# Kernel tuning notes

Measured on AMD Instinct MI355X. Metric: run time of the kernel, lower is better.

Reference implementation:

```python
import jax, jax.numpy as jnp
import numpy as np

B, D, L = 16, 256, 200
T = 1000   # max_frame_length
K = 3      # kernel_size
DW, DC = 4, 2


def setup_inputs() -> dict:
    key = jax.random.key(0)
    ks = jax.random.split(key, 16)
    plen = jax.random.randint(ks[0], (B,), 150, L + 1)
    pm = jnp.arange(L)[None, :] < plen[:, None]              # (B,L) True=valid
    phoneme_mask = pm[:, None, :]                            # (B,1,L)
    durations = jax.random.uniform(ks[1], (B, L), minval=1.0, maxval=8.0) * pm
    phoneme = jax.random.normal(ks[2], (B, D, L), dtype=jnp.float32)
    s = 0.05
    params = {
        'Wpw': jax.random.normal(ks[3], (D, D)) * s, 'bpw': jnp.zeros((D,)),
        'Cw': jax.random.normal(ks[4], (8, D, K)) * s, 'cbw': jnp.zeros((8,)),
        'Mw': jax.random.normal(ks[5], (10, DW)) * s, 'mbw': jnp.zeros((DW,)),
        'Lw': jax.random.normal(ks[6], (DW * D, D)) * s, 'lbw': jnp.zeros((D,)),
        'Wpc': jax.random.normal(ks[7], (D, D)) * s, 'bpc': jnp.zeros((D,)),
        'Cc': jax.random.normal(ks[8], (8, D, K)) * s, 'cbc': jnp.zeros((8,)),
        'Mc': jax.random.normal(ks[9], (10, DC)) * s, 'mbc': jnp.zeros((DC,)),
        'Lc': jax.random.normal(ks[10], (DW * DC, D)) * s, 'lbc': jnp.zeros((D,)),
        'Wo': jax.random.normal(ks[11], (D, 2 * D)) * s, 'bo': jnp.zeros((2 * D,)),
    }
    return {'durations': durations, 'phoneme': phoneme, 'phoneme_mask': phoneme_mask, **params}


def _conv_swish(x, W1, b1, Ck, cb, pm):
    # 1x1 conv (proj) then kernel-K 'same' conv then SiLU; mask padded phones
    h = jnp.einsum('od,bdl->bol', W1, x) + b1[None, :, None]
    h = jax.lax.conv_general_dilated(h, Ck, (1,), 'SAME',
                                     dimension_numbers=('NCH', 'OIH', 'NCH')) + cb[None, :, None]
    h = jax.nn.silu(h)
    h = jnp.where(pm[:, None, :], h, 0.0)
    return h.transpose(0, 2, 1)  # (B, L, 8)


def _mlp(S, E, h, M, mb):
    # concat start/end boundary scalars with per-phone conv features -> (B,T,L,10)
    feat = jnp.concatenate([S[..., None], E[..., None],
                            jnp.broadcast_to(h[:, None], (B, T, L, 8))], axis=-1)
    return jax.nn.silu(feat @ M + mb)


def _forward(durations, phoneme, phoneme_mask, Wpw, bpw, Cw, cbw, Mw, mbw, Lw, lbw,
             Wpc, bpc, Cc, cbc, Mc, mbc, Lc, lbc, Wo, bo):
    pm = phoneme_mask[:, 0, :]                                          # (B,L)
    frame_lengths = jnp.clip(jnp.round(durations.sum(-1)).astype(jnp.int32), 0, T)
    frame_mask = jnp.arange(T)[None, :] < frame_lengths[:, None]        # (B,T)
    attn_mask = frame_mask[:, :, None] & pm[:, None, :]                 # (B,T,L)
    sd = jnp.cumsum(durations, axis=-1)                                 # (B,L)
    sk = sd - durations
    t = jnp.arange(1, T + 1, dtype=durations.dtype)
    S = jnp.where(attn_mask, t[None, :, None] - sk[:, None, :], 0.0)    # (B,T,L)
    E = jnp.where(attn_mask, (sd - sk)[:, None, :], 0.0)                # (B,T,L)

    h_w = _conv_swish(phoneme, Wpw, bpw, Cw, cbw, pm)
    w = _mlp(S, E, h_w, Mw, mbw)                                        # (B,T,L,DW)
    w = jnp.where(pm[:, None, :, None], w, -jnp.inf)
    w = jax.nn.softmax(w, axis=2)                                       # softmax over phones
    w = jnp.where(frame_mask[:, :, None, None], w, 0.0)

    h_c = _conv_swish(phoneme, Wpc, bpc, Cc, cbc, pm)
    c = _mlp(S, E, h_c, Mc, mbc)                                        # (B,T,L,DC)

    wh = jnp.einsum('btlq,bdl->btqd', w, phoneme).reshape(B, T, DW * D) @ Lw + lbw
    wc = jnp.einsum('btlq,btlp->btqp', w, c).reshape(B, T, DW * DC) @ Lc + lbc
    whc = jnp.where(frame_mask[..., None], wh + wc, 0.0)                # (B,T,D)
    out = (whc @ Wo + bo).transpose(0, 2, 1)                            # (B,2D,T)
    return out, frame_mask, frame_lengths, w.transpose(0, 3, 1, 2)


def reference(durations, phoneme, phoneme_mask, Wpw, bpw, Cw, cbw, Mw, mbw, Lw, lbw,
              Wpc, bpc, Cc, cbc, Mc, mbc, Lc, lbc, Wo, bo):
    out, frame_mask, frame_lengths, w = _forward(
        durations, phoneme, phoneme_mask, Wpw, bpw, Cw, cbw, Mw, mbw, Lw, lbw,
        Wpc, bpc, Cc, cbc, Mc, mbc, Lc, lbc, Wo, bo)
    mean, log_std = jnp.split(out, 2, axis=1)                           # (B,D,T) each
    return (mean, log_std, frame_mask, frame_lengths, w)
```

## Files before the change

### kernel.cpp

```cpp
#include <hip/hip_runtime.h>
#include <hip/hip_bf16.h>
#include <math.h>

#define NB 16
#define ND 256
#define NL 200
#define NT 1000

typedef unsigned short ushort_t;
typedef __bf16 bf16x8 __attribute__((ext_vector_type(8)));
typedef float f32x4 __attribute__((ext_vector_type(4)));

#define LDS_AS(p) ((__attribute__((address_space(3))) void*)(p))
#define GLB_AS(p) ((const __attribute__((address_space(1))) void*)(p))

#define OFF_PHT   0u
#define OFF_SK    4966400u
#define OFF_EW    4969600u
#define OFF_EC    4975744u
#define OFF_BW2   4981888u
#define OFF_BC2   4981912u
#define OFF_FL    4981936u
#define OFF_GT    11535552u
#define OFF_WHC   13173952u
#define OFF_WOT   15221952u
#define OFF_BASE  15287488u
#define OFF_PHTB  15320256u
#define OFF_LWT   15844544u

__device__ __forceinline__ float silu_f(float x){ return x / (1.f + __expf(-x)); }
__device__ __forceinline__ ushort_t f2bf(float x){
  __hip_bfloat16 h = __float2bfloat16(x);
  return *(ushort_t*)&h;
}

__global__ __launch_bounds__(256) void k_stage1(
    const float* __restrict__ dur, const float* __restrict__ ph,
    const float* __restrict__ Wp_w, const float* __restrict__ C_w, const float* __restrict__ bp_w,
    const float* __restrict__ Wp_c, const float* __restrict__ C_c, const float* __restrict__ bp_c,
    const float* __restrict__ Wo, const float* __restrict__ Lw,
    float* __restrict__ sk_ws, int* __restrict__ fl_ws,
    float* __restrict__ o_fm, float* __restrict__ o_fl,
    float* __restrict__ Ew, float* __restrict__ Ec,
    float* __restrict__ bw2, float* __restrict__ bc2,
    ushort_t* __restrict__ WoT, ushort_t* __restrict__ LwT,
    float* __restrict__ phT, ushort_t* __restrict__ phTb)
{
  int bid = blockIdx.x, tid = threadIdx.x;
  if (bid < 16){
    int b = bid;
    __shared__ float sdur[NL];
    __shared__ float ssk[NL];
    __shared__ int sfl;
    if (tid < NL) sdur[tid] = dur[b*NL + tid];
    __syncthreads();
    if (tid == 0){
      float run = 0.f;
      for (int l = 0; l < NL; ++l){ ssk[l] = run; run += sdur[l]; }
      int fl = (int)rintf(run);
      fl = fl < 0 ? 0 : (fl > NT ? NT : fl);
      sfl = fl; fl_ws[b] = fl; o_fl[b] = (float)fl;
    }
    __syncthreads();
    if (tid < NL) sk_ws[b*NL + tid] = ssk[tid];
    for (int t = tid; t < NT; t += 256) o_fm[b*NT + t] = (t < sfl) ? 1.f : 0.f;
  } else if (bid < 1600){
    int sbid = bid - 16;
    if (sbid < 48){
      int gid = sbid*256 + tid;
      int branch = gid / 6144;
      int r = gid % 6144;
      int d = r & 255;
      int ock = r >> 8;
      int oc = ock / 3, k = ock % 3;
      const float* Wp = branch ? Wp_c : Wp_w;
      const float* C  = branch ? C_c  : C_w;
      float acc = 0.f;
      for (int i = 0; i < ND; ++i) acc += C[(oc*ND + i)*3 + k] * Wp[i*ND + d];
      (branch ? Ec : Ew)[r] = acc;
      if (d == 0){
        const float* bp = branch ? bp_c : bp_w;
        float bb = 0.f;
        for (int i = 0; i < ND; ++i) bb += C[(oc*ND + i)*3 + k] * bp[i];
        (branch ? bc2 : bw2)[ock] = bb;
      }
    } else {
      int gid = (sbid - 48)*256 + tid;
      if (gid < 131072){
        int n = gid >> 8, k = gid & 255;
        WoT[gid] = f2bf(Wo[(size_t)k*512 + n]);
      } else {
        int r = gid - 131072;
        int d = r & 255;
        int qn = r >> 8;
        int q = qn >> 8, n = qn & 255;
        LwT[r] = f2bf(Lw[((size_t)q*256 + d)*256 + n]);
      }
    }
  } else {
    int r = bid - 1600;
    int xb = r & 7, yb = (r >> 3) & 7, b = r >> 6;
    int l0 = xb*32, d0 = yb*32;
    int tx = tid & 31, ty = tid >> 5;
    __shared__ float tile[32][33];
    #pragma unroll
    for (int i = 0; i < 4; ++i){
      int d = d0 + ty + i*8, l = l0 + tx;
      tile[ty + i*8][tx] = (l < NL) ? ph[((size_t)b*ND + d)*NL + l] : 0.f;
    }
    __syncthreads();
    #pragma unroll
    for (int i = 0; i < 4; ++i){
      int l = l0 + ty + i*8, d = d0 + tx;
      float v = tile[tx][ty + i*8];
      if (l < NL) phT[((size_t)b*NL + l)*ND + d] = v;
      phTb[((size_t)b*256 + l)*ND + d] = f2bf(v);
    }
  }
}

__global__ __launch_bounds__(256) void k_stage2(
    const float* __restrict__ phT,
    const float* __restrict__ dur, const float* __restrict__ sk_ws,
    const float* __restrict__ Ew, const float* __restrict__ Ec,
    const float* __restrict__ bw2, const float* __restrict__ bc2,
    const float* __restrict__ cbw, const float* __restrict__ cbc,
    const float* __restrict__ Mw, const float* __restrict__ mbw,
    const float* __restrict__ Mc, const float* __restrict__ mbc,
    float4* __restrict__ base,
    const ushort_t* __restrict__ LwT, const ushort_t* __restrict__ phTb,
    ushort_t* __restrict__ Gt)
{
  int bid = blockIdx.x, tid = threadIdx.x;
  if (bid < 256){
    int b = bid >> 4, x = bid & 15;
    if (x >= 13){
      int l0 = 208 + (x - 13)*16;
      if (tid < 32)
        base[((size_t)(b*256 + l0 + (tid >> 1)))*2 + (tid & 1)] = make_float4(0,0,0,0);
      return;
    }
    __shared__ float sh[16][17];
    int lu = tid >> 4, u = tid & 15;
    int l = x*16 + lu;
    float h = 0.f;
    if (l < NL){
      int branch = u >> 3, oc = u & 7;
      const float* E  = branch ? Ec  : Ew;
      const float* b2 = branch ? bc2 : bw2;
      float val = (branch ? cbc : cbw)[oc];
      #pragma unroll
      for (int k = 0; k < 3; ++k){
        int ll = l + k - 1;
        if (ll < 0 || ll >= NL) continue;
        float acc = b2[oc*3 + k];
        const float4* Er = (const float4*)(E + (oc*3 + k)*ND);
        const float4* pr = (const float4*)(phT + ((size_t)b*NL + ll)*ND);
        #pragma unroll 8
        for (int d = 0; d < 64; ++d){
          float4 e = Er[d], p = pr[d];
          acc += e.x*p.x + e.y*p.y + e.z*p.z + e.w*p.w;
        }
        val += acc;
      }
      float pm = (dur[b*NL + l] > 0.5f) ? 1.f : 0.f;
      h = silu_f(val) * pm;
    }
    sh[lu][u] = h;
    __syncthreads();
    if (tid < 16){
      int ll = x*16 + tid;
      float4 o0 = make_float4(0,0,0,0);
      float4 o1 = make_float4(0,0,0,0);
      if (ll < NL){
        float dl  = dur[b*NL + ll];
        float pm  = (dl > 0.5f) ? 1.f : 0.f;
        float skl = sk_ws[b*NL + ll];
        float c1[4], c2[2];
        #pragma unroll
        for (int q = 0; q < 4; ++q) c1[q] = mbw[q] + dl*Mw[4 + q] - skl*Mw[q];
        #pragma unroll
        for (int p = 0; p < 2; ++p) c2[p] = mbc[p] + dl*Mc[2 + p] - skl*Mc[p];
        #pragma unroll
        for (int j = 0; j < 8; ++j){
          float hwv = sh[tid][j], hcv = sh[tid][8 + j];
          #pragma unroll
          for (int q = 0; q < 4; ++q) c1[q] += hwv*Mw[(2 + j)*4 + q];
          #pragma unroll
          for (int p = 0; p < 2; ++p) c2[p] += hcv*Mc[(2 + j)*2 + p];
        }
        o0 = make_float4(c1[0], c1[1], c1[2], c1[3]);
        o1 = make_float4(c2[0], c2[1], pm, 0.f);
      }
      base[((size_t)(b*256 + ll))*2 + 0] = o0;
      base[((size_t)(b*256 + ll))*2 + 1] = o1;
    }
  } else {
    int r = bid - 256;
    int xb = r & 1, yb = (r >> 1) & 1, bq = r >> 2;
    int b = bq >> 2, q = bq & 3;
    int m0 = yb * 128;
    int n0 = xb * 128;
    int lane = tid & 63, wave = tid >> 6;
    int wm = wave >> 1, wn = wave & 1;
    int col = lane & 15, kg4 = lane >> 4;
    f32x4 acc[4][4] = {};
    for (int kt = 0; kt < 8; ++kt){
      int k0 = kt*32;
      bf16x8 afr[4], bfr[4];
      #pragma unroll
      for (int i = 0; i < 4; ++i)
        afr[i] = *(const bf16x8*)(LwT + ((size_t)(q*256 + m0 + wm*64 + i*16 + col))*256 + k0 + kg4*8);
      #pragma unroll
      for (int j = 0; j < 4; ++j)
        bfr[j] = *(const bf16x8*)(phTb + ((size_t)(b*256 + n0 + wn*64 + j*16 + col))*256 + k0 + kg4*8);
      #pragma unroll
      for (int i = 0; i < 4; ++i)
        #pragma unroll
        for (int j = 0; j < 4; ++j)
          acc[i][j] = __builtin_amdgcn_mfma_f32_16x16x32_bf16(afr[i], bfr[j], acc[i][j], 0, 0, 0);
    }
    int rq = lane >> 4;
    #pragma unroll
    for (int i = 0; i < 4; ++i){
      #pragma unroll
      for (int rr = 0; rr < 4; ++rr){
        int n = m0 + wm*64 + i*16 + rq*4 + rr;
        #pragma unroll
        for (int j = 0; j < 4; ++j){
          int l = n0 + wn*64 + j*16 + col;
          if (l < NL)
            Gt[((size_t)b*ND + n)*800 + q*NL + l] = f2bf(acc[i][j][rr]);
        }
      }
    }
  }
}

#define AP 808
__global__ __launch_bounds__(256) void k_wv_fused(
    const float4* __restrict__ base,
    const int* __restrict__ fl_ws,
    const float* __restrict__ Mw, const float* __restrict__ Mc,
    const ushort_t* __restrict__ Gt,
    const float* __restrict__ Lc,
    const float* __restrict__ lbc,
    const float* __restrict__ lbw,
    float* __restrict__ wout,
    ushort_t* __restrict__ whc)
{
  __shared__ ushort_t As[32*AP];
  __shared__ float    wcs[32][8];
  int b = blockIdx.y;
  int m0 = blockIdx.x * 32;
  int tid = threadIdx.x, lane = tid & 63, wave = tid >> 6;
  int col = lane & 15, kg4 = lane >> 4;
  int fl = fl_ws[b];

  for (int s = 0; s < 8; ++s){
    int tl = wave*8 + s;
    int t = m0 + tl;
    if (t >= fl){
      for (int k = lane; k < 800; k += 64) As[tl*AP + k] = 0;
      if (lane < 8) wcs[tl][lane] = 0.f;
      if (t < NT){
        #pragma unroll
        for (int q = 0; q < 4; ++q)
          #pragma unroll
          for (int c = 0; c < 4; ++c){
            int l = c*64 + lane;
            if (l < NL) wout[(((size_t)(b*4 + q))*NT + t)*NL + l] = 0.f;
          }
      }
      continue;
    }
    float t1 = (float)(t + 1);
    float tqw[4], tqc[2];
    #pragma unroll
    for (int q = 0; q < 4; ++q) tqw[q] = t1 * Mw[q];
    #pragma unroll
    for (int p = 0; p < 2; ++p) tqc[p] = t1 * Mc[p];
    float z[4][4], cv[4][2], msk[4];
    float m[4] = {-INFINITY, -INFINITY, -INFINITY, -INFINITY};
    #pragma unroll
    for (int c = 0; c < 4; ++c){
      int l = c*64 + lane;
      float4 b0 = base[((size_t)(b*256 + l))*2 + 0];
      float4 b1 = base[((size_t)(b*256 + l))*2 + 1];
      float pm = b1.z;
      msk[c] = pm;
      float zz[4] = { b0.x + tqw[0], b0.y + tqw[1], b0.z + tqw[2], b0.w + tqw[3] };
      #pragma unroll
      for (int q = 0; q < 4; ++q){
        float sv = silu_f(zz[q]);
        z[c][q] = (pm > 0.f) ? sv : -INFINITY;
        m[q] = fmaxf(m[q], z[c][q]);
      }
      cv[c][0] = silu_f(b1.x + tqc[0]);
      cv[c][1] = silu_f(b1.y + tqc[1]);
    }
    #pragma unroll
    for (int q = 0; q < 4; ++q){
      float v = m[q];
      #pragma unroll
      for (int off = 32; off; off >>= 1) v = fmaxf(v, __shfl_xor(v, off));
      m[q] = v;
    }
    float s4[4] = {0,0,0,0};
    #pragma unroll
    for (int c = 0; c < 4; ++c){
      #pragma unroll
      for (int q = 0; q < 4; ++q){
        float e = (msk[c] > 0.f) ? __expf(z[c][q] - m[q]) : 0.f;
        z[c][q] = e;
        s4[q] += e;
      }
    }
    #pragma unroll
    for (int q = 0; q < 4; ++q){
      float v = s4[q];
      #pragma unroll
      for (int off = 32; off; off >>= 1) v += __shfl_xor(v, off);
      s4[q] = 1.f / v;
    }
    float wc[8] = {0,0,0,0,0,0,0,0};
    #pragma unroll
    for (int c = 0; c < 4; ++c){
      int l = c*64 + lane;
      bool lv = l < NL;
      #pragma unroll
      for (int q = 0; q < 4; ++q){
        float wq = z[c][q] * s4[q];
        if (lv){
          wout[(((size_t)(b*4 + q))*NT + t)*NL + l] = wq;
          As[tl*AP + q*NL + l] = f2bf(wq);
        }
        wc[q*2 + 0] += wq * cv[c][0];
        wc[q*2 + 1] += wq * cv[c][1];
      }
    }
    #pragma unroll
    for (int u = 0; u < 8; ++u){
      float v = wc[u];
      #pragma unroll
      for (int off = 32; off; off >>= 1) v += __shfl_xor(v, off);
      wc[u] = v;
    }
    if (lane == 0){
      #pragma unroll
      for (int u = 0; u < 8; ++u) wcs[tl][u] = wc[u];
    }
  }
  __syncthreads();

  f32x4 acc[2][4] = {};
  const ushort_t* Gb = Gt + (size_t)b*ND*800;
  for (int kt = 0; kt < 25; ++kt){
    int k0 = kt*32;
    bf16x8 afr[2], bfr[4];
    #pragma unroll
    for (int i = 0; i < 2; ++i)
      afr[i] = *(const bf16x8*)(&As[(i*16 + col)*AP + k0 + kg4*8]);
    #pragma unroll
    for (int j = 0; j < 4; ++j)
      bfr[j] = *(const bf16x8*)(Gb + ((size_t)(wave*64 + j*16 + col))*800 + k0 + kg4*8);
    #pragma unroll
    for (int i = 0; i < 2; ++i)
      #pragma unroll
      for (int j = 0; j < 4; ++j)
        acc[i][j] = __builtin_amdgcn_mfma_f32_16x16x32_bf16(afr[i], bfr[j], acc[i][j], 0, 0, 0);
  }

  int rq = lane >> 4;
  float lcn[4][8], lbn[4], lbwn[4];
  #pragma unroll
  for (int j = 0; j < 4; ++j){
    int n = wave*64 + j*16 + col;
    lbn[j] = lbc[n]; lbwn[j] = lbw[n];
    #pragma unroll
    for (int u = 0; u < 8; ++u) lcn[j][u] = Lc[u*ND + n];
  }
  #pragma unroll
  for (int i = 0; i < 2; ++i){
    #pragma unroll
    for (int r = 0; r < 4; ++r){
      int tl = i*16 + rq*4 + r;
      int t = m0 + tl;
      if (t >= NT) continue;
      float f = (t < fl) ? 1.f : 0.f;
      #pragma unroll
      for (int j = 0; j < 4; ++j){
        float vcv = lbn[j]
          + wcs[tl][0]*lcn[j][0] + wcs[tl][1]*lcn[j][1]
          + wcs[tl][2]*lcn[j][2] + wcs[tl][3]*lcn[j][3]
          + wcs[tl][4]*lcn[j][4] + wcs[tl][5]*lcn[j][5]
          + wcs[tl][6]*lcn[j][6] + wcs[tl][7]*lcn[j][7];
        int n = wave*64 + j*16 + col;
        whc[((size_t)b*NT + t)*ND + n] = f2bf(f * (acc[i][j][r] + lbwn[j] + vcv));
      }
    }
  }
}

__global__ __launch_bounds__(256) void k_gemmO_mfma(
    const ushort_t* __restrict__ whc,
    const ushort_t* __restrict__ WoT,
    const float* __restrict__ bo,
    float* __restrict__ o_mean, float* __restrict__ o_lstd)
{
  int m0 = blockIdx.y * 128;
  int n0 = blockIdx.x * 128;
  int tid = threadIdx.x, lane = tid & 63, wave = tid >> 6;
  int wm = wave >> 1, wn = wave & 1;
  int col = lane & 15, kg4 = lane >> 4;

  f32x4 acc[4][4] = {};

  for (int kt = 0; kt < 8; ++kt){
    int k0 = kt*32;
    bf16x8 afr[4], bfr[4];
    #pragma unroll
    for (int i = 0; i < 4; ++i)
      afr[i] = *(const bf16x8*)(WoT + ((size_t)(m0 + wm*64 + i*16 + col))*ND + k0 + kg4*8);
    #pragma unroll
    for (int j = 0; j < 4; ++j)
      bfr[j] = *(const bf16x8*)(whc + ((size_t)(n0 + wn*64 + j*16 + col))*ND + k0 + kg4*8);
    #pragma unroll
    for (int i = 0; i < 4; ++i)
      #pragma unroll
      for (int j = 0; j < 4; ++j)
        acc[i][j] = __builtin_amdgcn_mfma_f32_16x16x32_bf16(afr[i], bfr[j], acc[i][j], 0, 0, 0);
  }

  int rq = lane >> 4;
  #pragma unroll
  for (int i = 0; i < 4; ++i){
    #pragma unroll
    for (int r = 0; r < 4; ++r){
      int s = m0 + wm*64 + i*16 + rq*4 + r;
      float bov = bo[s];
      #pragma unroll
      for (int j = 0; j < 4; ++j){
        int bt = n0 + wn*64 + j*16 + col;
        int b = bt / NT, t = bt - b*NT;
        float v = acc[i][j][r] + bov;
        if (s < ND) o_mean[((size_t)b*ND + s)*NT + t] = v;
        else        o_lstd[((size_t)b*ND + (s - ND))*NT + t] = v;
      }
    }
  }
}

extern "C" void kernel_launch(void* const* d_in, const int* in_sizes, int n_in,
                              void* d_out, int out_size, void* d_ws, size_t ws_size,
                              hipStream_t stream)
{
  const float* dur = (const float*)d_in[0];
  const float* ph  = (const float*)d_in[1];
  const float* Wpw = (const float*)d_in[3];
  const float* bpw = (const float*)d_in[4];
  const float* Cw  = (const float*)d_in[5];
  const float* cbw = (const float*)d_in[6];
  const float* Mw  = (const float*)d_in[7];
  const float* mbw = (const float*)d_in[8];
  const float* Lw  = (const float*)d_in[9];
  const float* lbw = (const float*)d_in[10];
  const float* Wpc = (const float*)d_in[11];
  const float* bpc = (const float*)d_in[12];
  const float* Cc  = (const float*)d_in[13];
  const float* cbc = (const float*)d_in[14];
  const float* Mc  = (const float*)d_in[15];
  const float* mbc = (const float*)d_in[16];
  const float* Lc  = (const float*)d_in[17];
  const float* lbc = (const float*)d_in[18];
  const float* Wo  = (const float*)d_in[19];
  const float* bo  = (const float*)d_in[20];

  float* out    = (float*)d_out;
  float* o_mean = out;
  float* o_lstd = out + (size_t)NB*ND*NT;
  float* o_fm   = o_lstd + (size_t)NB*ND*NT;
  float* o_fl   = o_fm + NB*NT;
  float* o_w    = o_fl + NB;

  float* ws   = (float*)d_ws;
  float* phT  = ws + OFF_PHT;
  float* sk   = ws + OFF_SK;
  float* Ew   = ws + OFF_EW;
  float* Ec   = ws + OFF_EC;
  float* bw2  = ws + OFF_BW2;
  float* bc2  = ws + OFF_BC2;
  int*   fl   = (int*)(ws + OFF_FL);
  ushort_t* Gt   = (ushort_t*)(ws + OFF_GT);
  ushort_t* whc  = (ushort_t*)(ws + OFF_WHC);
  ushort_t* WoT  = (ushort_t*)(ws + OFF_WOT);
  float4*   base = (float4*)(ws + OFF_BASE);
  ushort_t* phTb = (ushort_t*)(ws + OFF_PHTB);
  ushort_t* LwT  = (ushort_t*)(ws + OFF_LWT);

  k_stage1<<<2624, 256, 0, stream>>>(dur, ph, Wpw, Cw, bpw, Wpc, Cc, bpc, Wo, Lw,
                                     sk, fl, o_fm, o_fl, Ew, Ec, bw2, bc2,
                                     WoT, LwT, phT, phTb);
  k_stage2<<<512, 256, 0, stream>>>(phT, dur, sk, Ew, Ec, bw2, bc2, cbw, cbc,
                                    Mw, mbw, Mc, mbc, base, LwT, phTb, Gt);
  {
    dim3 g(32, NB);
    k_wv_fused<<<g, 256, 0, stream>>>(base, fl, Mw, Mc, Gt, Lc, lbc, lbw,
                                      o_w, whc);
  }
  {
    dim3 g(125, 4);
    k_gemmO_mfma<<<g, 256, 0, stream>>>(whc, WoT, bo, o_mean, o_lstd);
  }
}
```

Before: 254.2 us.

## Fuse four kernel launches into one persistent kernel with grid barriers

Merges the four stage kernels into a single persistent kernel of 512 blocks that separates stages with a software grid-wide barrier built on atomics, and adds a memset to reset the barrier counter before each launch. Stage 1 work is spread over the blocks with a grid-stride loop. The aim is to remove per-launch overhead and the gaps between kernels. The risks are a deadlock if all 512 blocks cannot be resident at once (the code requests 2 blocks per CU through launch bounds and uses about 52 KB of shared memory per block), the cost of the barrier spin itself, and lost occupancy in later stages where only some blocks have work.

```diff
diff --git a/kernel.cpp b/kernel.cpp
--- a/kernel.cpp
+++ b/kernel.cpp
@@ -6,13 +6,12 @@
 #define ND 256
 #define NL 200
 #define NT 1000
+#define NBLK 512
+#define AP 808
 
 typedef unsigned short ushort_t;
 typedef __bf16 bf16x8 __attribute__((ext_vector_type(8)));
 typedef float f32x4 __attribute__((ext_vector_type(4)));
-
-#define LDS_AS(p) ((__attribute__((address_space(3))) void*)(p))
-#define GLB_AS(p) ((const __attribute__((address_space(1))) void*)(p))
 
 #define OFF_PHT   0u
 #define OFF_SK    4966400u
@@ -21,6 +20,7 @@
 #define OFF_BW2   4981888u
 #define OFF_BC2   4981912u
 #define OFF_FL    4981936u
+#define OFF_BAR   4982000u
 #define OFF_GT    11535552u
 #define OFF_WHC   13173952u
 #define OFF_WOT   15221952u
@@ -34,166 +34,186 @@
   return *(ushort_t*)&h;
 }
 
-__global__ __launch_bounds__(256) void k_stage1(
+__device__ __forceinline__ void grid_sync(unsigned* bar){
+  __syncthreads();
+  if (threadIdx.x == 0){
+    __threadfence();
+    unsigned g = __hip_atomic_load(bar + 1, __ATOMIC_RELAXED, __HIP_MEMORY_SCOPE_AGENT);
+    unsigned my = __hip_atomic_fetch_add(bar, 1u, __ATOMIC_ACQ_REL, __HIP_MEMORY_SCOPE_AGENT);
+    if (my == (unsigned)(NBLK - 1)){
+      __hip_atomic_store(bar, 0u, __ATOMIC_RELAXED, __HIP_MEMORY_SCOPE_AGENT);
+      __hip_atomic_fetch_add(bar + 1, 1u, __ATOMIC_RELEASE, __HIP_MEMORY_SCOPE_AGENT);
+    } else {
+      while (__hip_atomic_load(bar + 1, __ATOMIC_ACQUIRE, __HIP_MEMORY_SCOPE_AGENT) == g)
+        __builtin_amdgcn_s_sleep(2);
+    }
+    __threadfence();
+  }
+  __syncthreads();
+}
+
+__global__ __launch_bounds__(256, 2) void k_all(
     const float* __restrict__ dur, const float* __restrict__ ph,
     const float* __restrict__ Wp_w, const float* __restrict__ C_w, const float* __restrict__ bp_w,
     const float* __restrict__ Wp_c, const float* __restrict__ C_c, const float* __restrict__ bp_c,
     const float* __restrict__ Wo, const float* __restrict__ Lw,
+    const float* __restrict__ cbw, const float* __restrict__ cbc,
+    const float* __restrict__ Mw, const float* __restrict__ mbw,
+    const float* __restrict__ Mc, const float* __restrict__ mbc,
+    const float* __restrict__ Lc, const float* __restrict__ lbc,
+    const float* __restrict__ lbw, const float* __restrict__ bo,
     float* __restrict__ sk_ws, int* __restrict__ fl_ws,
     float* __restrict__ o_fm, float* __restrict__ o_fl,
     float* __restrict__ Ew, float* __restrict__ Ec,
     float* __restrict__ bw2, float* __restrict__ bc2,
     ushort_t* __restrict__ WoT, ushort_t* __restrict__ LwT,
-    float* __restrict__ phT, ushort_t* __restrict__ phTb)
+    float* __restrict__ phT, ushort_t* __restrict__ phTb,
+    float4* __restrict__ base, ushort_t* __restrict__ Gt,
+    float* __restrict__ wout, ushort_t* __restrict__ whc,
+    float* __restrict__ o_mean, float* __restrict__ o_lstd,
+    unsigned* __restrict__ bar)
 {
+  __shared__ __align__(16) unsigned char smem[52736];
   int bid = blockIdx.x, tid = threadIdx.x;
-  if (bid < 16){
-    int b = bid;
-    __shared__ float sdur[NL];
-    __shared__ float ssk[NL];
-    __shared__ int sfl;
-    if (tid < NL) sdur[tid] = dur[b*NL + tid];
+
+  for (int vb = bid; vb < 2624; vb += NBLK){
+    if (vb < 16){
+      int b = vb;
+      float* sdur = (float*)smem;
+      float* ssk  = sdur + 256;
+      int*   sfl  = (int*)(ssk + 256);
+      if (tid < NL) sdur[tid] = dur[b*NL + tid];
+      __syncthreads();
+      if (tid == 0){
+        float run = 0.f;
+        for (int l = 0; l < NL; ++l){ ssk[l] = run; run += sdur[l]; }
+        int fl = (int)rintf(run);
+        fl = fl < 0 ? 0 : (fl > NT ? NT : fl);
+        sfl[0] = fl; fl_ws[b] = fl; o_fl[b] = (float)fl;
+      }
+      __syncthreads();
+      if (tid < NL) sk_ws[b*NL + tid] = ssk[tid];
+      int flv = sfl[0];
+      for (int t = tid; t < NT; t += 256) o_fm[b*NT + t] = (t < flv) ? 1.f : 0.f;
+    } else if (vb < 1600){
+      int sbid = vb - 16;
+      if (sbid < 48){
+        int gid = sbid*256 + tid;
+        int branch = gid / 6144;
+        int r = gid % 6144;
+        int d = r & 255;
+        int ock = r >> 8;
+        int oc = ock / 3, k = ock % 3;
+        const float* Wp = branch ? Wp_c : Wp_w;
+        const float* C  = branch ? C_c  : C_w;
+        float acc = 0.f;
+        for (int i = 0; i < ND; ++i) acc += C[(oc*ND + i)*3 + k] * Wp[i*ND + d];
+        (branch ? Ec : Ew)[r] = acc;
+        if (d == 0){
+          const float* bp = branch ? bp_c : bp_w;
+          float bb = 0.f;
+          for (int i = 0; i < ND; ++i) bb += C[(oc*ND + i)*3 + k] * bp[i];
+          (branch ? bc2 : bw2)[ock] = bb;
+        }
+      } else {
+        int gid = (sbid - 48)*256 + tid;
+        if (gid < 131072){
+          int n = gid >> 8, k = gid & 255;
+          WoT[gid] = f2bf(Wo[(size_t)k*512 + n]);
+        } else {
+          int r = gid - 131072;
+          int d = r & 255;
+          int qn = r >> 8;
+          int q = qn >> 8, n = qn & 255;
+          LwT[r] = f2bf(Lw[((size_t)q*256 + d)*256 + n]);
+        }
+      }
+    } else {
+      int r = vb - 1600;
+      int xb = r & 7, yb = (r >> 3) & 7, b = r >> 6;
+      int l0 = xb*32, d0 = yb*32;
+      int tx = tid & 31, ty = tid >> 5;
+      float (*tile)[33] = (float (*)[33])smem;
+      #pragma unroll
+      for (int i = 0; i < 4; ++i){
+        int d = d0 + ty + i*8, l = l0 + tx;
+        tile[ty + i*8][tx] = (l < NL) ? ph[((size_t)b*ND + d)*NL + l] : 0.f;
+      }
+      __syncthreads();
+      #pragma unroll
+      for (int i = 0; i < 4; ++i){
+        int l = l0 + ty + i*8, d = d0 + tx;
+        float v = tile[tx][ty + i*8];
+        if (l < NL) phT[((size_t)b*NL + l)*ND + d] = v;
+        phTb[((size_t)b*256 + l)*ND + d] = f2bf(v);
+      }
+    }
     __syncthreads();
-    if (tid == 0){
-      float run = 0.f;
-      for (int l = 0; l < NL; ++l){ ssk[l] = run; run += sdur[l]; }
-      int fl = (int)rintf(run);
-      fl = fl < 0 ? 0 : (fl > NT ? NT : fl);
-      sfl = fl; fl_ws[b] = fl; o_fl[b] = (float)fl;
-    }
-    __syncthreads();
-    if (tid < NL) sk_ws[b*NL + tid] = ssk[tid];
-    for (int t = tid; t < NT; t += 256) o_fm[b*NT + t] = (t < sfl) ? 1.f : 0.f;
-  } else if (bid < 1600){
-    int sbid = bid - 16;
-    if (sbid < 48){
-      int gid = sbid*256 + tid;
-      int branch = gid / 6144;
-      int r = gid % 6144;
-      int d = r & 255;
-      int ock = r >> 8;
-      int oc = ock / 3, k = ock % 3;
-      const float* Wp = branch ? Wp_c : Wp_w;
-      const float* C  = branch ? C_c  : C_w;
-      float acc = 0.f;
-      for (int i = 0; i < ND; ++i) acc += C[(oc*ND + i)*3 + k] * Wp[i*ND + d];
-      (branch ? Ec : Ew)[r] = acc;
-      if (d == 0){
-        const float* bp = branch ? bp_c : bp_w;
-        float bb = 0.f;
-        for (int i = 0; i < ND; ++i) bb += C[(oc*ND + i)*3 + k] * bp[i];
-        (branch ? bc2 : bw2)[ock] = bb;
-      }
-    } else {
-      int gid = (sbid - 48)*256 + tid;
-      if (gid < 131072){
-        int n = gid >> 8, k = gid & 255;
-        WoT[gid] = f2bf(Wo[(size_t)k*512 + n]);
-      } else {
-        int r = gid - 131072;
-        int d = r & 255;
-        int qn = r >> 8;
-        int q = qn >> 8, n = qn & 255;
-        LwT[r] = f2bf(Lw[((size_t)q*256 + d)*256 + n]);
-      }
-    }
-  } else {
-    int r = bid - 1600;
-    int xb = r & 7, yb = (r >> 3) & 7, b = r >> 6;
-    int l0 = xb*32, d0 = yb*32;
-    int tx = tid & 31, ty = tid >> 5;
-    __shared__ float tile[32][33];
-    #pragma unroll
-    for (int i = 0; i < 4; ++i){
-      int d = d0 + ty + i*8, l = l0 + tx;
-      tile[ty + i*8][tx] = (l < NL) ? ph[((size_t)b*ND + d)*NL + l] : 0.f;
-    }
-    __syncthreads();
-    #pragma unroll
-    for (int i = 0; i < 4; ++i){
-      int l = l0 + ty + i*8, d = d0 + tx;
-      float v = tile[tx][ty + i*8];
-      if (l < NL) phT[((size_t)b*NL + l)*ND + d] = v;
-      phTb[((size_t)b*256 + l)*ND + d] = f2bf(v);
-    }
   }
-}
-
-__global__ __launch_bounds__(256) void k_stage2(
-    const float* __restrict__ phT,
-    const float* __restrict__ dur, const float* __restrict__ sk_ws,
-    const float* __restrict__ Ew, const float* __restrict__ Ec,
-    const float* __restrict__ bw2, const float* __restrict__ bc2,
-    const float* __restrict__ cbw, const float* __restrict__ cbc,
-    const float* __restrict__ Mw, const float* __restrict__ mbw,
-    const float* __restrict__ Mc, const float* __restrict__ mbc,
-    float4* __restrict__ base,
-    const ushort_t* __restrict__ LwT, const ushort_t* __restrict__ phTb,
-    ushort_t* __restrict__ Gt)
-{
-  int bid = blockIdx.x, tid = threadIdx.x;
+  grid_sync(bar);
+
   if (bid < 256){
     int b = bid >> 4, x = bid & 15;
     if (x >= 13){
       int l0 = 208 + (x - 13)*16;
       if (tid < 32)
         base[((size_t)(b*256 + l0 + (tid >> 1)))*2 + (tid & 1)] = make_float4(0,0,0,0);
-      return;
-    }
-    __shared__ float sh[16][17];
-    int lu = tid >> 4, u = tid & 15;
-    int l = x*16 + lu;
-    float h = 0.f;
-    if (l < NL){
-      int branch = u >> 3, oc = u & 7;
-      const float* E  = branch ? Ec  : Ew;
-      const float* b2 = branch ? bc2 : bw2;
-      float val = (branch ? cbc : cbw)[oc];
-      #pragma unroll
-      for (int k = 0; k < 3; ++k){
-        int ll = l + k - 1;
-        if (ll < 0 || ll >= NL) continue;
-        float acc = b2[oc*3 + k];
-        const float4* Er = (const float4*)(E + (oc*3 + k)*ND);
-        const float4* pr = (const float4*)(phT + ((size_t)b*NL + ll)*ND);
-        #pragma unroll 8
-        for (int d = 0; d < 64; ++d){
-          float4 e = Er[d], p = pr[d];
-          acc += e.x*p.x + e.y*p.y + e.z*p.z + e.w*p.w;
-        }
-        val += acc;
-      }
-      float pm = (dur[b*NL + l] > 0.5f) ? 1.f : 0.f;
-      h = silu_f(val) * pm;
-    }
-    sh[lu][u] = h;
-    __syncthreads();
-    if (tid < 16){
-      int ll = x*16 + tid;
-      float4 o0 = make_float4(0,0,0,0);
-      float4 o1 = make_float4(0,0,0,0);
-      if (ll < NL){
-        float dl  = dur[b*NL + ll];
-        float pm  = (dl > 0.5f) ? 1.f : 0.f;
-        float skl = sk_ws[b*NL + ll];
-        float c1[4], c2[2];
-        #pragma unroll
-        for (int q = 0; q < 4; ++q) c1[q] = mbw[q] + dl*Mw[4 + q] - skl*Mw[q];
-        #pragma unroll
-        for (int p = 0; p < 2; ++p) c2[p] = mbc[p] + dl*Mc[2 + p] - skl*Mc[p];
-        #pragma unroll
-        for (int j = 0; j < 8; ++j){
-          float hwv = sh[tid][j], hcv = sh[tid][8 + j];
+    } else {
+      float (*sh)[17] = (float (*)[17])smem;
+      int lu = tid >> 4, u = tid & 15;
+      int l = x*16 + lu;
+      float h = 0.f;
+      if (l < NL){
+        int branch = u >> 3, oc = u & 7;
+        const float* E  = branch ? Ec  : Ew;
+        const float* b2 = branch ? bc2 : bw2;
+        float val = (branch ? cbc : cbw)[oc];
+        #pragma unroll
+        for (int k = 0; k < 3; ++k){
+          int ll = l + k - 1;
+          if (ll < 0 || ll >= NL) continue;
+          float acc = b2[oc*3 + k];
+          const float4* Er = (const float4*)(E + (oc*3 + k)*ND);
+          const float4* pr = (const float4*)(phT + ((size_t)b*NL + ll)*ND);
+          #pragma unroll 8
+          for (int d = 0; d < 64; ++d){
+            float4 e = Er[d], p = pr[d];
+            acc += e.x*p.x + e.y*p.y + e.z*p.z + e.w*p.w;
+          }
+          val += acc;
+        }
+        float pm = (dur[b*NL + l] > 0.5f) ? 1.f : 0.f;
+        h = silu_f(val) * pm;
+      }
+      sh[lu][u] = h;
+      __syncthreads();
+      if (tid < 16){
+        int ll = x*16 + tid;
+        float4 o0 = make_float4(0,0,0,0);
+        float4 o1 = make_float4(0,0,0,0);
+        if (ll < NL){
+          float dl  = dur[b*NL + ll];
+          float pm  = (dl > 0.5f) ? 1.f : 0.f;
+          float skl = sk_ws[b*NL + ll];
+          float c1[4], c2[2];
           #pragma unroll
-          for (int q = 0; q < 4; ++q) c1[q] += hwv*Mw[(2 + j)*4 + q];
+          for (int q = 0; q < 4; ++q) c1[q] = mbw[q] + dl*Mw[4 + q] - skl*Mw[q];
           #pragma unroll
-          for (int p = 0; p < 2; ++p) c2[p] += hcv*Mc[(2 + j)*2 + p];
-        }
-        o0 = make_float4(c1[0], c1[1], c1[2], c1[3]);
-        o1 = make_float4(c2[0], c2[1], pm, 0.f);
-      }
-      base[((size_t)(b*256 + ll))*2 + 0] = o0;
-      base[((size_t)(b*256 + ll))*2 + 1] = o1;
+          for (int p = 0; p < 2; ++p) c2[p] = mbc[p] + dl*Mc[2 + p] - skl*Mc[p];
+          #pragma unroll
+          for (int j = 0; j < 8; ++j){
+            float hwv = sh[tid][j], hcv = sh[tid][8 + j];
+            #pragma unroll
+            for (int q = 0; q < 4; ++q) c1[q] += hwv*Mw[(2 + j)*4 + q];
+            #pragma unroll
+            for (int p = 0; p < 2; ++p) c2[p] += hcv*Mc[(2 + j)*2 + p];
+          }
+          o0 = make_float4(c1[0], c1[1], c1[2], c1[3]);
+          o1 = make_float4(c2[0], c2[1], pm, 0.f);
+        }
+        base[((size_t)(b*256 + ll))*2 + 0] = o0;
+        base[((size_t)(b*256 + ll))*2 + 1] = o1;
+      }
     }
   } else {
     int r = bid - 256;
@@ -235,217 +255,203 @@
       }
     }
   }
-}
-
-#define AP 808
-__global__ __launch_bounds__(256) void k_wv_fused(
-    const float4* __restrict__ base,
-    const int* __restrict__ fl_ws,
-    const float* __restrict__ Mw, const float* __restrict__ Mc,
-    const ushort_t* __restrict__ Gt,
-    const float* __restrict__ Lc,
-    const float* __restrict__ lbc,
-    const float* __restrict__ lbw,
-    float* __restrict__ wout,
-    ushort_t* __restrict__ whc)
-{
-  __shared__ ushort_t As[32*AP];
-  __shared__ float    wcs[32][8];
-  int b = blockIdx.y;
-  int m0 = blockIdx.x * 32;
-  int tid = threadIdx.x, lane = tid & 63, wave = tid >> 6;
-  int col = lane & 15, kg4 = lane >> 4;
-  int fl = fl_ws[b];
-
-  for (int s = 0; s < 8; ++s){
-    int tl = wave*8 + s;
-    int t = m0 + tl;
-    if (t >= fl){
-      for (int k = lane; k < 800; k += 64) As[tl*AP + k] = 0;
-      if (lane < 8) wcs[tl][lane] = 0.f;
-      if (t < NT){
-        #pragma unroll
-        for (int q = 0; q < 4; ++q)
+  grid_sync(bar);
+
+  {
+    ushort_t* As = (ushort_t*)smem;
+    float (*wcs)[8] = (float (*)[8])(smem + 32*AP*2);
+    int b = bid >> 5;
+    int m0 = (bid & 31) * 32;
+    int lane = tid & 63, wave = tid >> 6;
+    int col = lane & 15, kg4 = lane >> 4;
+    int fl = fl_ws[b];
+
+    for (int s = 0; s < 8; ++s){
+      int tl = wave*8 + s;
+      int t = m0 + tl;
+      if (t >= fl){
+        for (int k = lane; k < 800; k += 64) As[tl*AP + k] = 0;
+        if (lane < 8) wcs[tl][lane] = 0.f;
+        if (t < NT){
           #pragma unroll
-          for (int c = 0; c < 4; ++c){
-            int l = c*64 + lane;
-            if (l < NL) wout[(((size_t)(b*4 + q))*NT + t)*NL + l] = 0.f;
+          for (int q = 0; q < 4; ++q)
+            #pragma unroll
+            for (int c = 0; c < 4; ++c){
+              int l = c*64 + lane;
+              if (l < NL) wout[(((size_t)(b*4 + q))*NT + t)*NL + l] = 0.f;
+            }
+        }
+        continue;
+      }
+      float t1 = (float)(t + 1);
+      float tqw[4], tqc[2];
+      #pragma unroll
+      for (int q = 0; q < 4; ++q) tqw[q] = t1 * Mw[q];
+      #pragma unroll
+      for (int p = 0; p < 2; ++p) tqc[p] = t1 * Mc[p];
+      float z[4][4], cv[4][2], msk[4];
+      float m[4] = {-INFINITY, -INFINITY, -INFINITY, -INFINITY};
+      #pragma unroll
+      for (int c = 0; c < 4; ++c){
+        int l = c*64 + lane;
+        float4 b0 = base[((size_t)(b*256 + l))*2 + 0];
+        float4 b1 = base[((size_t)(b*256 + l))*2 + 1];
+        float pm = b1.z;
+        msk[c] = pm;
+        float zz[4] = { b0.x + tqw[0], b0.y + tqw[1], b0.z + tqw[2], b0.w + tqw[3] };
+        #pragma unroll
+        for (int q = 0; q < 4; ++q){
+          float sv = silu_f(zz[q]);
+          z[c][q] = (pm > 0.f) ? sv : -INFINITY;
+          m[q] = fmaxf(m[q], z[c][q]);
+        }
+        cv[c][0] = silu_f(b1.x + tqc[0]);
+        cv[c][1] = silu_f(b1.y + tqc[1]);
+      }
+      #pragma unroll
+      for (int q = 0; q < 4; ++q){
+        float v = m[q];
+        #pragma unroll
+        for (int off = 32; off; off >>= 1) v = fmaxf(v, __shfl_xor(v, off));
+        m[q] = v;
+      }
+      float s4[4] = {0,0,0,0};
+      #pragma unroll
+      for (int c = 0; c < 4; ++c){
+        #pragma unroll
+        for (int q = 0; q < 4; ++q){
+          float e = (msk[c] > 0.f) ? __expf(z[c][q] - m[q]) : 0.f;
+          z[c][q] = e;
+          s4[q] += e;
+        }
+      }
+      #pragma unroll
+      for (int q = 0; q < 4; ++q){
+        float v = s4[q];
+        #pragma unroll
+        for (int off = 32; off; off >>= 1) v += __shfl_xor(v, off);
+        s4[q] = 1.f / v;
+      }
+      float wc[8] = {0,0,0,0,0,0,0,0};
+      #pragma unroll
+      for (int c = 0; c < 4; ++c){
+        int l = c*64 + lane;
+        bool lv = l < NL;
+        #pragma unroll
+        for (int q = 0; q < 4; ++q){
+          float wq = z[c][q] * s4[q];
+          if (lv){
+            wout[(((size_t)(b*4 + q))*NT + t)*NL + l] = wq;
+            As[tl*AP + q*NL + l] = f2bf(wq);
           }
-      }
-      continue;
-    }
-    float t1 = (float)(t + 1);
-    float tqw[4], tqc[2];
+          wc[q*2 + 0] += wq * cv[c][0];
+          wc[q*2 + 1] += wq * cv[c][1];
+        }
+      }
+      #pragma unroll
+      for (int u = 0; u < 8; ++u){
+        float v = wc[u];
+        #pragma unroll
+        for (int off = 32; off; off >>= 1) v += __shfl_xor(v, off);
+        wc[u] = v;
+      }
+      if (lane == 0){
+        #pragma unroll
+        for (int u = 0; u < 8; ++u) wcs[tl][u] = wc[u];
+      }
+    }
+    __syncthreads();
+
+    f32x4 acc[2][4] = {};
+    const ushort_t* Gb = Gt + (size_t)b*ND*800;
+    for (int kt = 0; kt < 25; ++kt){
+      int k0 = kt*32;
+      bf16x8 afr[2], bfr[4];
+      #pragma unroll
+      for (int i = 0; i < 2; ++i)
+        afr[i] = *(const bf16x8*)(&As[(i*16 + col)*AP + k0 + kg4*8]);
+      #pragma unroll
+      for (int j = 0; j < 4; ++j)
+        bfr[j] = *(const bf16x8*)(Gb + ((size_t)(wave*64 + j*16 + col))*800 + k0 + kg4*8);
+      #pragma unroll
+      for (int i = 0; i < 2; ++i)
+        #pragma unroll
+        for (int j = 0; j < 4; ++j)
+          acc[i][j] = __builtin_amdgcn_mfma_f32_16x16x32_bf16(afr[i], bfr[j], acc[i][j], 0, 0, 0);
+    }
+
+    int rq = lane >> 4;
+    float lcn[4][8], lbn[4], lbwn[4];
     #pragma unroll
-    for (int q = 0; q < 4; ++q) tqw[q] = t1 * Mw[q];
+    for (int j = 0; j < 4; ++j){
+      int n = wave*64 + j*16 + col;
+      lbn[j] = lbc[n]; lbwn[j] = lbw[n];
+      #pragma unroll
+      for (int u = 0; u < 8; ++u) lcn[j][u] = Lc[u*ND + n];
+    }
     #pragma unroll
-    for (int p = 0; p < 2; ++p) tqc[p] = t1 * Mc[p];
-    float z[4][4], cv[4][2], msk[4];
-    float m[4] = {-INFINITY, -INFINITY, -INFINITY, -INFINITY};
+    for (int i = 0; i < 2; ++i){
+      #pragma unroll
+      for (int r = 0; r < 4; ++r){
+        int tl = i*16 + rq*4 + r;
+        int t = m0 + tl;
+        if (t >= NT) continue;
+        float f = (t < fl) ? 1.f : 0.f;
+        #pragma unroll
+        for (int j = 0; j < 4; ++j){
+          float vcv = lbn[j]
+            + wcs[tl][0]*lcn[j][0] + wcs[tl][1]*lcn[j][1]
+            + wcs[tl][2]*lcn[j][2] + wcs[tl][3]*lcn[j][3]
+            + wcs[tl][4]*lcn[j][4] + wcs[tl][5]*lcn[j][5]
+            + wcs[tl][6]*lcn[j][6] + wcs[tl][7]*lcn[j][7];
+          int n = wave*64 + j*16 + col;
+          whc[((size_t)b*NT + t)*ND + n] = f2bf(f * (acc[i][j][r] + lbwn[j] + vcv));
+        }
+      }
+    }
+  }
+  grid_sync(bar);
+
+  if (bid < 500){
+    int m0 = (bid / 125) * 128;
+    int n0 = (bid % 125) * 128;
+    int lane = tid & 63, wave = tid >> 6;
+    int wm = wave >> 1, wn = wave & 1;
+    int col = lane & 15, kg4 = lane >> 4;
+
+    f32x4 acc[4][4] = {};
+
+    for (int kt = 0; kt < 8; ++kt){
+      int k0 = kt*32;
+      bf16x8 afr[4], bfr[4];
+      #pragma unroll
+      for (int i = 0; i < 4; ++i)
+        afr[i] = *(const bf16x8*)(WoT + ((size_t)(m0 + wm*64 + i*16 + col))*ND + k0 + kg4*8);
+      #pragma unroll
+      for (int j = 0; j < 4; ++j)
+        bfr[j] = *(const bf16x8*)(whc + ((size_t)(n0 + wn*64 + j*16 + col))*ND + k0 + kg4*8);
+      #pragma unroll
+      for (int i = 0; i < 4; ++i)
+        #pragma unroll
+        for (int j = 0; j < 4; ++j)
+          acc[i][j] = __builtin_amdgcn_mfma_f32_16x16x32_bf16(afr[i], bfr[j], acc[i][j], 0, 0, 0);
+    }
+
+    int rq = lane >> 4;
     #pragma unroll
-    for (int c = 0; c < 4; ++c){
-      int l = c*64 + lane;
-      float4 b0 = base[((size_t)(b*256 + l))*2 + 0];
-      float4 b1 = base[((size_t)(b*256 + l))*2 + 1];
-      float pm = b1.z;
-      msk[c] = pm;
-      float zz[4] = { b0.x + tqw[0], b0.y + tqw[1], b0.z + tqw[2], b0.w + tqw[3] };
-      #pragma unroll
-      for (int q = 0; q < 4; ++q){
-        float sv = silu_f(zz[q]);
-        z[c][q] = (pm > 0.f) ? sv : -INFINITY;
-        m[q] = fmaxf(m[q], z[c][q]);
-      }
-      cv[c][0] = silu_f(b1.x + tqc[0]);
-      cv[c][1] = silu_f(b1.y + tqc[1]);
-    }
-    #pragma unroll
-    for (int q = 0; q < 4; ++q){
-      float v = m[q];
-      #pragma unroll
-      for (int off = 32; off; off >>= 1) v = fmaxf(v, __shfl_xor(v, off));
-      m[q] = v;
-    }
-    float s4[4] = {0,0,0,0};
-    #pragma unroll
-    for (int c = 0; c < 4; ++c){
-      #pragma unroll
-      for (int q = 0; q < 4; ++q){
-        float e = (msk[c] > 0.f) ? __expf(z[c][q] - m[q]) : 0.f;
-        z[c][q] = e;
-        s4[q] += e;
-      }
-    }
-    #pragma unroll
-    for (int q = 0; q < 4; ++q){
-      float v = s4[q];
-      #pragma unroll
-      for (int off = 32; off; off >>= 1) v += __shfl_xor(v, off);
-      s4[q] = 1.f / v;
-    }
-    float wc[8] = {0,0,0,0,0,0,0,0};
-    #pragma unroll
-    for (int c = 0; c < 4; ++c){
-      int l = c*64 + lane;
-      bool lv = l < NL;
-      #pragma unroll
-      for (int q = 0; q < 4; ++q){
-        float wq = z[c][q] * s4[q];
-        if (lv){
-          wout[(((size_t)(b*4 + q))*NT + t)*NL + l] = wq;
-          As[tl*AP + q*NL + l] = f2bf(wq);
-        }
-        wc[q*2 + 0] += wq * cv[c][0];
-        wc[q*2 + 1] += wq * cv[c][1];
-      }
-    }
-    #pragma unroll
-    for (int u = 0; u < 8; ++u){
-      float v = wc[u];
-      #pragma unroll
-      for (int off = 32; off; off >>= 1) v += __shfl_xor(v, off);
-      wc[u] = v;
-    }
-    if (lane == 0){
-      #pragma unroll
-      for (int u = 0; u < 8; ++u) wcs[tl][u] = wc[u];
-    }
-  }
-  __syncthreads();
-
-  f32x4 acc[2][4] = {};
-  const ushort_t* Gb = Gt + (size_t)b*ND*800;
-  for (int kt = 0; kt < 25; ++kt){
-    int k0 = kt*32;
-    bf16x8 afr[2], bfr[4];
-    #pragma unroll
-    for (int i = 0; i < 2; ++i)
-      afr[i] = *(const bf16x8*)(&As[(i*16 + col)*AP + k0 + kg4*8]);
-    #pragma unroll
-    for (int j = 0; j < 4; ++j)
-      bfr[j] = *(const bf16x8*)(Gb + ((size_t)(wave*64 + j*16 + col))*800 + k0 + kg4*8);
-    #pragma unroll
-    for (int i = 0; i < 2; ++i)
-      #pragma unroll
-      for (int j = 0; j < 4; ++j)
-        acc[i][j] = __builtin_amdgcn_mfma_f32_16x16x32_bf16(afr[i], bfr[j], acc[i][j], 0, 0, 0);
-  }
-
-  int rq = lane >> 4;
-  float lcn[4][8], lbn[4], lbwn[4];
-  #pragma unroll
-  for (int j = 0; j < 4; ++j){
-    int n = wave*64 + j*16 + col;
-    lbn[j] = lbc[n]; lbwn[j] = lbw[n];
-    #pragma unroll
-    for (int u = 0; u < 8; ++u) lcn[j][u] = Lc[u*ND + n];
-  }
-  #pragma unroll
-  for (int i = 0; i < 2; ++i){
-    #pragma unroll
-    for (int r = 0; r < 4; ++r){
-      int tl = i*16 + rq*4 + r;
-      int t = m0 + tl;
-      if (t >= NT) continue;
-      float f = (t < fl) ? 1.f : 0.f;
-      #pragma unroll
-      for (int j = 0; j < 4; ++j){
-        float vcv = lbn[j]
-          + wcs[tl][0]*lcn[j][0] + wcs[tl][1]*lcn[j][1]
-          + wcs[tl][2]*lcn[j][2] + wcs[tl][3]*lcn[j][3]
-          + wcs[tl][4]*lcn[j][4] + wcs[tl][5]*lcn[j][5]
-          + wcs[tl][6]*lcn[j][6] + wcs[tl][7]*lcn[j][7];
-        int n = wave*64 + j*16 + col;
-        whc[((size_t)b*NT + t)*ND + n] = f2bf(f * (acc[i][j][r] + lbwn[j] + vcv));
-      }
-    }
-  }
-}
-
-__global__ __launch_bounds__(256) void k_gemmO_mfma(
-    const ushort_t* __restrict__ whc,
-    const ushort_t* __restrict__ WoT,
-    const float* __restrict__ bo,
-    float* __restrict__ o_mean, float* __restrict__ o_lstd)
-{
-  int m0 = blockIdx.y * 128;
-  int n0 = blockIdx.x * 128;
-  int tid = threadIdx.x, lane = tid & 63, wave = tid >> 6;
-  int wm = wave >> 1, wn = wave & 1;
-  int col = lane & 15, kg4 = lane >> 4;
-
-  f32x4 acc[4][4] = {};
-
-  for (int kt = 0; kt < 8; ++kt){
-    int k0 = kt*32;
-    bf16x8 afr[4], bfr[4];
-    #pragma unroll
-    for (int i = 0; i < 4; ++i)
-      afr[i] = *(const bf16x8*)(WoT + ((size_t)(m0 + wm*64 + i*16 + col))*ND + k0 + kg4*8);
-    #pragma unroll
-    for (int j = 0; j < 4; ++j)
-      bfr[j] = *(const bf16x8*)(whc + ((size_t)(n0 + wn*64 + j*16 + col))*ND + k0 + kg4*8);
-    #pragma unroll
-    for (int i = 0; i < 4; ++i)
-      #pragma unroll
-      for (int j = 0; j < 4; ++j)
-        acc[i][j] = __builtin_amdgcn_mfma_f32_16x16x32_bf16(afr[i], bfr[j], acc[i][j], 0, 0, 0);
-  }
-
-  int rq = lane >> 4;
-  #pragma unroll
-  for (int i = 0; i < 4; ++i){
-    #pragma unroll
-    for (int r = 0; r < 4; ++r){
-      int s = m0 + wm*64 + i*16 + rq*4 + r;
-      float bov = bo[s];
-      #pragma unroll
-      for (int j = 0; j < 4; ++j){
-        int bt = n0 + wn*64 + j*16 + col;
-        int b = bt / NT, t = bt - b*NT;
-        float v = acc[i][j][r] + bov;
-        if (s < ND) o_mean[((size_t)b*ND + s)*NT + t] = v;
-        else        o_lstd[((size_t)b*ND + (s - ND))*NT + t] = v;
+    for (int i = 0; i < 4; ++i){
+      #pragma unroll
+      for (int r = 0; r < 4; ++r){
+        int s = m0 + wm*64 + i*16 + rq*4 + r;
+        float bov = bo[s];
+        #pragma unroll
+        for (int j = 0; j < 4; ++j){
+          int bt = n0 + wn*64 + j*16 + col;
+          int b = bt / NT, t = bt - b*NT;
+          float v = acc[i][j][r] + bov;
+          if (s < ND) o_mean[((size_t)b*ND + s)*NT + t] = v;
+          else        o_lstd[((size_t)b*ND + (s - ND))*NT + t] = v;
+        }
       }
     }
   }
@@ -491,6 +497,7 @@
   float* bw2  = ws + OFF_BW2;
   float* bc2  = ws + OFF_BC2;
   int*   fl   = (int*)(ws + OFF_FL);
+  unsigned* bar = (unsigned*)(ws + OFF_BAR);
   ushort_t* Gt   = (ushort_t*)(ws + OFF_GT);
   ushort_t* whc  = (ushort_t*)(ws + OFF_WHC);
   ushort_t* WoT  = (ushort_t*)(ws + OFF_WOT);
@@ -498,18 +505,12 @@
   ushort_t* phTb = (ushort_t*)(ws + OFF_PHTB);
   ushort_t* LwT  = (ushort_t*)(ws + OFF_LWT);
 
-  k_stage1<<<2624, 256, 0, stream>>>(dur, ph, Wpw, Cw, bpw, Wpc, Cc, bpc, Wo, Lw,
-                                     sk, fl, o_fm, o_fl, Ew, Ec, bw2, bc2,
-                                     WoT, LwT, phT, phTb);
-  k_stage2<<<512, 256, 0, stream>>>(phT, dur, sk, Ew, Ec, bw2, bc2, cbw, cbc,
-                                    Mw, mbw, Mc, mbc, base, LwT, phTb, Gt);
-  {
-    dim3 g(32, NB);
-    k_wv_fused<<<g, 256, 0, stream>>>(base, fl, Mw, Mc, Gt, Lc, lbc, lbw,
-                                      o_w, whc);
-  }
-  {
-    dim3 g(125, 4);
-    k_gemmO_mfma<<<g, 256, 0, stream>>>(whc, WoT, bo, o_mean, o_lstd);
-  }
+  hipMemsetAsync(bar, 0, 2*sizeof(unsigned), stream);
+
+  k_all<<<NBLK, 256, 0, stream>>>(
+      dur, ph, Wpw, Cw, bpw, Wpc, Cc, bpc, Wo, Lw,
+      cbw, cbc, Mw, mbw, Mc, mbc, Lc, lbc, lbw, bo,
+      sk, fl, o_fm, o_fl, Ew, Ec, bw2, bc2,
+      WoT, LwT, phT, phTb, base, Gt, o_w, whc,
+      o_mean, o_lstd, bar);
 }
```

After: 863.5 us. 240% more time.
